# Kernel optimization log

Measured on AMD Instinct MI355X. Metric: run time of the kernel, lower is better.

Reference implementation:

```python
import jax, jax.numpy as jnp
import numpy as np

B, H0, W0, DIM, HEADS, WS, SHIFT = 32, 56, 56, 384, 12, 7, 3
MLP_HID = DIM * 4
N = WS * WS  # tokens per window

def _rel_pos_index(ws):
    coords = np.stack(np.meshgrid(np.arange(ws), np.arange(ws), indexing='ij')).reshape(2, -1)
    rel = (coords[:, :, None] - coords[:, None, :]).transpose(1, 2, 0)
    rel[:, :, 0] += ws - 1
    rel[:, :, 1] += ws - 1
    rel[:, :, 0] *= 2 * ws - 1
    return rel.sum(-1)  # (N, N) int

REL_IDX = _rel_pos_index(WS)

def _shift_mask(H, W, ws, shift):
    # standard Swin SW-MSA mask: 0 within same region, -100 across regions
    img = np.zeros((H, W), dtype=np.int32)
    cnt = 0
    for hs in (slice(0, -ws), slice(-ws, -shift), slice(-shift, None)):
        for wsl in (slice(0, -ws), slice(-ws, -shift), slice(-shift, None)):
            img[hs, wsl] = cnt
            cnt += 1
    mw = img.reshape(H // ws, ws, W // ws, ws).transpose(0, 2, 1, 3).reshape(-1, ws * ws)
    return np.where(mw[:, None, :] != mw[:, :, None], -100.0, 0.0).astype(np.float32)  # (nW, N, N)

MASK = _shift_mask(H0, W0, WS, SHIFT)

def _ln(x, g, b, eps=1e-5):
    m = x.mean(-1, keepdims=True)
    v = ((x - m) ** 2).mean(-1, keepdims=True)
    return (x - m) / jnp.sqrt(v + eps) * g + b

def setup_inputs():
    key = jax.random.key(0)
    ks = jax.random.split(key, 8)
    d = {}
    d['x'] = jax.random.normal(ks[0], (B, H0 * W0, DIM), jnp.float32)
    d['H'], d['W'] = H0, W0
    d['norm1_g'] = jnp.ones((DIM,), jnp.float32)
    d['norm1_b'] = jnp.zeros((DIM,), jnp.float32)
    d['qkv_w'] = jax.random.normal(ks[1], (3 * DIM, DIM), jnp.float32) * 0.02
    d['qkv_b'] = jnp.zeros((3 * DIM,), jnp.float32)
    d['rpb_table'] = jax.random.normal(ks[2], ((2 * WS - 1) ** 2, HEADS), jnp.float32) * 0.02
    d['proj_w'] = jax.random.normal(ks[3], (DIM, DIM), jnp.float32) * 0.02
    d['proj_b'] = jnp.zeros((DIM,), jnp.float32)
    d['norm2_g'] = jnp.ones((DIM,), jnp.float32)
    d['norm2_b'] = jnp.zeros((DIM,), jnp.float32)
    d['fc1_w'] = jax.random.normal(ks[4], (MLP_HID, DIM), jnp.float32) * 0.02
    d['fc1_b'] = jnp.zeros((MLP_HID,), jnp.float32)
    d['fc2_w'] = jax.random.normal(ks[5], (DIM, MLP_HID), jnp.float32) * 0.02
    d['fc2_b'] = jnp.zeros((DIM,), jnp.float32)
    return d

def reference(x, H, W, norm1_g, norm1_b, qkv_w, qkv_b, rpb_table, proj_w, proj_b, norm2_g, norm2_b, fc1_w, fc1_b, fc2_w, fc2_b):
    Bx, L, C = x.shape
    hd = C // HEADS
    scale = hd ** -0.5
    shortcut = x
    xn = _ln(x, norm1_g, norm1_b).reshape(Bx, H, W, C)
    if SHIFT > 0:
        xn = jnp.roll(xn, (-SHIFT, -SHIFT), axis=(1, 2))
    nWh, nWw = H // WS, W // WS
    nW = nWh * nWw
    # window partition: (B, H, W, C) -> (B*nW, N, C)
    xw = xn.reshape(Bx, nWh, WS, nWw, WS, C).transpose(0, 1, 3, 2, 4, 5).reshape(-1, N, C)
    qkv = (xw @ qkv_w.T + qkv_b).reshape(-1, N, 3, HEADS, hd).transpose(2, 0, 3, 1, 4)
    q, k, v = qkv[0] * scale, qkv[1], qkv[2]  # (B*nW, HEADS, N, hd)
    attn = jnp.einsum('bhnd,bhmd->bhnm', q, k)
    bias = rpb_table[jnp.asarray(REL_IDX.reshape(-1))].reshape(N, N, HEADS).transpose(2, 0, 1)
    attn = attn + bias[None]
    if SHIFT > 0:
        attn = attn.reshape(Bx, nW, HEADS, N, N) + jnp.asarray(MASK)[None, :, None]
        attn = attn.reshape(-1, HEADS, N, N)
    attn = jax.nn.softmax(attn, axis=-1)
    out = jnp.einsum('bhnm,bhmd->bhnd', attn, v).transpose(0, 2, 1, 3).reshape(-1, N, C)
    out = out @ proj_w.T + proj_b
    # window reverse: (B*nW, N, C) -> (B, H, W, C)
    xr = out.reshape(Bx, nWh, nWw, WS, WS, C).transpose(0, 1, 3, 2, 4, 5).reshape(Bx, H, W, C)
    if SHIFT > 0:
        xr = jnp.roll(xr, (SHIFT, SHIFT), axis=(1, 2))
    x = shortcut + xr.reshape(Bx, L, C)
    h = _ln(x, norm2_g, norm2_b)
    h = jax.nn.gelu(h @ fc1_w.T + fc1_b, approximate=False)  # nn.GELU default = exact erf
    h = h @ fc2_w.T + fc2_b
    return x + h
```

## Files before the change

kernel.cpp:

```cpp
#include <hip/hip_runtime.h>
#include <hip/hip_bf16.h>

#define C_DIM   384
#define HEADS   12
#define HDIM    32
#define NTOK    49
#define TOT_WIN 2048
#define M_TOK   100352
#define QKV_N   1152
#define MLP_N   1536
#define SHIFT_V 3

typedef __bf16 bf16x8_t __attribute__((ext_vector_type(8)));
typedef float  f32x4_t  __attribute__((ext_vector_type(4)));

__device__ inline float b2f(ushort u) {
    union { unsigned u; float f; } p; p.u = ((unsigned)u) << 16; return p.f;
}
__device__ inline ushort f2b(float f) {
    union { float f; unsigned u; } p; p.f = f;
    unsigned r = p.u + 0x7FFF + ((p.u >> 16) & 1);
    return (ushort)(r >> 16);
}
__device__ inline float ldin(const void* p, size_t i, int dt) {
    return dt ? b2f(((const ushort*)p)[i]) : ((const float*)p)[i];
}

__device__ inline void gload_lds16(const ushort* g, ushort* l) {
    __builtin_amdgcn_global_load_lds(
        (__attribute__((address_space(1))) void*)const_cast<ushort*>(g),
        (__attribute__((address_space(3))) void*)l, 16, 0, 0);
}

__device__ inline int win2tok(int grow) {
    int widx = grow / 49, tok = grow - widx * 49;
    int b = widx >> 6, w_ = widx & 63;
    int wh = w_ >> 3, ww = w_ & 7;
    int r = tok / 7, c = tok - r * 7;
    int h = wh * 7 + r + SHIFT_V; if (h >= 56) h -= 56;
    int wc = ww * 7 + c + SHIFT_V; if (wc >= 56) wc -= 56;
    return b * 3136 + h * 56 + wc;
}

__global__ void sniff_kernel(const ushort* x16, int* flag) {
    const int tid = threadIdx.x;
    int cnt = 0;
    for (int i = tid; i < 4096; i += 256) {
        ushort u = x16[2 * i];
        int e = (u >> 7) & 0xFF;
        if ((u & 0x7FFF) == 0 || (e >= 107 && e <= 147)) cnt++;
    }
    __shared__ int ss[256];
    ss[tid] = cnt; __syncthreads();
    for (int s = 128; s; s >>= 1) { if (tid < s) ss[tid] += ss[tid + s]; __syncthreads(); }
    if (tid == 0) *flag = (ss[0] >= 2048) ? 1 : 0;
}

__global__ void cvt_w_kernel(const void* src, ushort* dst, int n, const int* flagp) {
    const int dt = *flagp;
    for (int i = blockIdx.x * blockDim.x + threadIdx.x; i < n; i += gridDim.x * blockDim.x)
        dst[i] = dt ? ((const ushort*)src)[i] : f2b(((const float*)src)[i]);
}

__global__ void cvt_p_kernel(const void* n1g, const void* n1b, const void* qkvb,
                             const void* projb, const void* n2g, const void* n2b,
                             const void* fc1b, const void* fc2b, const void* rpb,
                             float* prm, const int* flagp) {
    const int dt = *flagp;
    for (int i = threadIdx.x; i < 7020; i += 256) {
        float v;
        if      (i < 384)  v = ldin(n1g,  i,        dt);
        else if (i < 768)  v = ldin(n1b,  i - 384,  dt);
        else if (i < 1920) v = ldin(qkvb, i - 768,  dt);
        else if (i < 2304) v = ldin(projb,i - 1920, dt);
        else if (i < 2688) v = ldin(n2g,  i - 2304, dt);
        else if (i < 3072) v = ldin(n2b,  i - 2688, dt);
        else if (i < 4608) v = ldin(fc1b, i - 3072, dt);
        else if (i < 4992) v = ldin(fc2b, i - 4608, dt);
        else               v = ldin(rpb,  i - 4992, dt);
        prm[i] = v;
    }
}

template<int MODE>
__global__ __launch_bounds__(256) void ln_kernel(
    const void* __restrict__ x, const float* __restrict__ g,
    const float* __restrict__ b, ushort* __restrict__ out,
    const int* flagp, int moff)
{
    const int dt = *flagp;
    const int wid = threadIdx.x >> 6, lane = threadIdx.x & 63;
    const int m = blockIdx.x * 4 + wid;
    const int src = (MODE == 0) ? win2tok(moff + m) : (moff + m);

    float v[6]; float s = 0.f, sq = 0.f;
    #pragma unroll
    for (int k = 0; k < 6; ++k) {
        v[k] = ldin(x, (size_t)src * C_DIM + lane + 64 * k, dt);
        s += v[k]; sq += v[k] * v[k];
    }
    #pragma unroll
    for (int off = 32; off; off >>= 1) {
        s  += __shfl_xor(s,  off, 64);
        sq += __shfl_xor(sq, off, 64);
    }
    float mean = s * (1.f / 384.f);
    float var  = sq * (1.f / 384.f) - mean * mean;
    float rstd = rsqrtf(var + 1e-5f);
    #pragma unroll
    for (int k = 0; k < 6; ++k) {
        int col = lane + 64 * k;
        out[(size_t)m * C_DIM + col] =
            f2b((v[k] - mean) * rstd * g[col] + b[col]);
    }
}

template<int MODE>
__global__ __launch_bounds__(256, 2) void gemm_bt(
    const ushort* __restrict__ A, const ushort* __restrict__ W,
    const float* __restrict__ bias, ushort* outb, void* outv,
    const void* resid, const int* flagp, int N, int K, int Mrows, int moff)
{
    __shared__ __align__(16) ushort As[2][128 * 32];
    __shared__ __align__(16) ushort Bs[2][128 * 32];

    const int dt   = *flagp;
    const int tid  = threadIdx.x;
    const int wid  = tid >> 6;
    const int lane = tid & 63;
    const int bm = blockIdx.x * 128;
    const int bn = blockIdx.y * 128;
    const int wm = (wid >> 1) * 64;
    const int wn = (wid & 1) * 64;
    const int lrow = lane & 15;
    const int lk   = (lane >> 4) << 3;

    const int c0    = wid * 2;
    const int srow0 = c0 * 16 + (lane >> 2);
    const int srow1 = srow0 + 16;
    const int skoff = (lane & 3) << 3;

    const int ar0 = (bm + srow0 < Mrows) ? (bm + srow0) : (Mrows - 1);
    const int ar1 = (bm + srow1 < Mrows) ? (bm + srow1) : (Mrows - 1);

    const ushort* pa0 = A + (size_t)ar0 * K + skoff;
    const ushort* pa1 = A + (size_t)ar1 * K + skoff;
    const ushort* pb0 = W + (size_t)(bn + srow0) * K + skoff;
    const ushort* pb1 = W + (size_t)(bn + srow1) * K + skoff;

    float biasf[4]; int coln[4];
    #pragma unroll
    for (int n = 0; n < 4; ++n) {
        coln[n] = bn + wn + n * 16 + lrow;
        biasf[n] = bias[coln[n]];
    }

    f32x4_t acc[4][4];
    #pragma unroll
    for (int m = 0; m < 4; ++m)
        #pragma unroll
        for (int n = 0; n < 4; ++n) acc[m][n] = (f32x4_t){0.f, 0.f, 0.f, 0.f};

    const int nk = K >> 5;
    gload_lds16(pa0, As[0] + (c0)     * 512);
    gload_lds16(pa1, As[0] + (c0 + 1) * 512);
    gload_lds16(pb0, Bs[0] + (c0)     * 512);
    gload_lds16(pb1, Bs[0] + (c0 + 1) * 512);

    int cur = 0;
    for (int kt = 0; kt < nk; ++kt) {
        if (kt + 1 < nk) {
            const int nxt = cur ^ 1;
            const int k1 = (kt + 1) << 5;
            gload_lds16(pa0 + k1, As[nxt] + (c0)     * 512);
            gload_lds16(pa1 + k1, As[nxt] + (c0 + 1) * 512);
            gload_lds16(pb0 + k1, Bs[nxt] + (c0)     * 512);
            gload_lds16(pb1 + k1, Bs[nxt] + (c0 + 1) * 512);
            __builtin_amdgcn_sched_barrier(0);
            asm volatile("s_waitcnt vmcnt(4)" ::: "memory");
        } else {
            asm volatile("s_waitcnt vmcnt(0)" ::: "memory");
        }
        __builtin_amdgcn_s_barrier();
        __builtin_amdgcn_sched_barrier(0);

        bf16x8_t af[4], bfr[4];
        #pragma unroll
        for (int m = 0; m < 4; ++m)
            af[m] = *(const bf16x8_t*)&As[cur][(wm + m * 16 + lrow) * 32 + lk];
        #pragma unroll
        for (int n = 0; n < 4; ++n)
            bfr[n] = *(const bf16x8_t*)&Bs[cur][(wn + n * 16 + lrow) * 32 + lk];
        #pragma unroll
        for (int m = 0; m < 4; ++m)
            #pragma unroll
            for (int n = 0; n < 4; ++n)
                acc[m][n] = __builtin_amdgcn_mfma_f32_16x16x32_bf16(
                    af[m], bfr[n], acc[m][n], 0, 0, 0);

        __builtin_amdgcn_sched_barrier(0);
        __builtin_amdgcn_s_barrier();
        cur ^= 1;
    }

    const int rbase = bm + wm + ((lane >> 4) << 2);
    #pragma unroll
    for (int m = 0; m < 4; ++m) {
        #pragma unroll
        for (int j = 0; j < 4; ++j) {
            int grow = rbase + m * 16 + j;
            if (grow >= Mrows) continue;
            #pragma unroll
            for (int n = 0; n < 4; ++n) {
                float v = acc[m][n][j] + biasf[n];
                if (MODE == 0) {
                    outb[(size_t)grow * N + coln[n]] = f2b(v);
                } else if (MODE == 2) {
                    v = 0.5f * v * (1.0f + erff(v * 0.70710678118654752f));
                    outb[(size_t)grow * N + coln[n]] = f2b(v);
                } else {
                    size_t orow = (MODE == 1) ? (size_t)win2tok(moff + grow)
                                              : (size_t)(moff + grow);
                    size_t oidx = orow * (size_t)N + coln[n];
                    float r = v + ldin(resid, oidx, dt);
                    if (dt) ((ushort*)outv)[oidx] = f2b(r);
                    else    ((float*) outv)[oidx] = r;
                }
            }
        }
    }
}

__global__ __launch_bounds__(256) void attn_kernel(
    const ushort* __restrict__ qkv, const float* __restrict__ rpb,
    ushort* __restrict__ out, int win_off)
{
    __shared__ __align__(16) ushort Pl[4][64 * 64];
    __shared__ __align__(16) ushort Vtl[4][32 * 64];

    const int tid = threadIdx.x, wid = tid >> 6, lane = tid & 63;
    const int lo = lane & 15, hi = lane >> 4;
    const int widx = blockIdx.x;
    const int w_ = (win_off + widx) & 63;
    const int wh = w_ >> 3, ww = w_ & 7;
    const bool edge = (wh == 7) || (ww == 7);

    char* P  = (char*)Pl[wid];
    char* Vw = (char*)Vtl[wid];

    int qr[4], qc[4], rq[4];
    #pragma unroll
    for (int n = 0; n < 4; ++n) {
        int q = n * 16 + lo; if (q > 48) q = 48;
        qr[n] = q / 7; qc[n] = q - qr[n] * 7;
        int gh = wh * 7 + qr[n], gw = ww * 7 + qc[n];
        rq[n] = (gh < 49 ? 0 : (gh < 53 ? 1 : 2)) * 3 + (gw < 49 ? 0 : (gw < 53 ? 1 : 2));
    }

    for (int h = wid; h < HEADS; h += 4) {
        const size_t hb = (size_t)widx * 49 * QKV_N + h * HDIM;

        bf16x8_t kf[4], qf[4];
        #pragma unroll
        for (int t = 0; t < 4; ++t) {
            int r = t * 16 + lo;
            bf16x8_t z = {};
            kf[t] = z; qf[t] = z;
            if (r < 49) {
                kf[t] = *(const bf16x8_t*)(qkv + hb + (size_t)r * QKV_N + 384 + hi * 8);
                qf[t] = *(const bf16x8_t*)(qkv + hb + (size_t)r * QKV_N + hi * 8);
            }
        }

        {
            const int kk = lane;
            union { bf16x8_t v; ushort u[8]; } vv[4];
            #pragma unroll
            for (int c = 0; c < 4; ++c) {
                bf16x8_t z = {};
                vv[c].v = (kk < 49) ? *(const bf16x8_t*)(qkv + hb + (size_t)kk * QKV_N + 768 + c * 8)
                                    : z;
            }
            #pragma unroll
            for (int d = 0; d < 32; ++d) {
                int byo = (d * 128 + kk * 2) ^ ((d & 7) << 4);
                *(ushort*)(Vw + byo) = vv[d >> 3].u[d & 7];
            }
        }

        f32x4_t St[4][4];
        #pragma unroll
        for (int m = 0; m < 4; ++m)
            #pragma unroll
            for (int n = 0; n < 4; ++n) St[m][n] = (f32x4_t){0.f, 0.f, 0.f, 0.f};
        #pragma unroll
        for (int m = 0; m < 4; ++m)
            #pragma unroll
            for (int n = 0; n < 4; ++n)
                St[m][n] = __builtin_amdgcn_mfma_f32_16x16x32_bf16(kf[m], qf[n], St[m][n], 0, 0, 0);

        #pragma unroll
        for (int m = 0; m < 4; ++m) {
            #pragma unroll
            for (int j = 0; j < 4; ++j) {
                const int kk = m * 16 + hi * 4 + j;
                const int kcl = (kk > 48) ? 48 : kk;
                const int kr = kcl / 7, kc = kcl - kr * 7;
                int rk = 0;
                if (edge) {
                    int gh = wh * 7 + kr, gw = ww * 7 + kc;
                    rk = (gh < 49 ? 0 : (gh < 53 ? 1 : 2)) * 3 + (gw < 49 ? 0 : (gw < 53 ? 1 : 2));
                }
                #pragma unroll
                for (int n = 0; n < 4; ++n) {
                    int idx = (qr[n] - kr + 6) * 13 + (qc[n] - kc + 6);
                    float v = St[m][n][j] * 0.17677669529663687f + rpb[idx * 12 + h];
                    if (edge && (rq[n] != rk)) v -= 100.f;
                    if (kk > 48) v = -1e30f;
                    St[m][n][j] = v;
                }
            }
        }

        float sm[4];
        #pragma unroll
        for (int n = 0; n < 4; ++n) {
            float mv = St[0][n][0];
            #pragma unroll
            for (int m = 0; m < 4; ++m)
                #pragma unroll
                for (int j = 0; j < 4; ++j) mv = fmaxf(mv, St[m][n][j]);
            mv = fmaxf(mv, __shfl_xor(mv, 16, 64));
            mv = fmaxf(mv, __shfl_xor(mv, 32, 64));
            float sv = 0.f;
            #pragma unroll
            for (int m = 0; m < 4; ++m)
                #pragma unroll
                for (int j = 0; j < 4; ++j) {
                    float e = __expf(St[m][n][j] - mv);
                    St[m][n][j] = e; sv += e;
                }
            sv += __shfl_xor(sv, 16, 64);
            sv += __shfl_xor(sv, 32, 64);
            sm[n] = 1.f / sv;
        }

        #pragma unroll
        for (int m = 0; m < 4; ++m) {
            #pragma unroll
            for (int n = 0; n < 4; ++n) {
                union { ushort4 u4; __bf16 b[4]; } pk;
                #pragma unroll
                for (int j = 0; j < 4; ++j) pk.b[j] = (__bf16)(St[m][n][j] * sm[n]);
                int byo = ((n * 16 + lo) * 128 + (m * 16 + hi * 4) * 2) ^ ((lo & 7) << 4);
                *(ushort4*)(P + byo) = pk.u4;
            }
        }

        f32x4_t Oa[4][2];
        #pragma unroll
        for (int mt = 0; mt < 4; ++mt)
            #pragma unroll
            for (int nt = 0; nt < 2; ++nt) Oa[mt][nt] = (f32x4_t){0.f, 0.f, 0.f, 0.f};
        #pragma unroll
        for (int s = 0; s < 2; ++s) {
            bf16x8_t vf[2];
            #pragma unroll
            for (int nt = 0; nt < 2; ++nt) {
                int byo = ((nt * 16 + lo) * 128 + s * 64 + hi * 16) ^ ((lo & 7) << 4);
                vf[nt] = *(const bf16x8_t*)(Vw + byo);
            }
            #pragma unroll
            for (int mt = 0; mt < 4; ++mt) {
                int byo = ((mt * 16 + lo) * 128 + s * 64 + hi * 16) ^ ((lo & 7) << 4);
                bf16x8_t pf = *(const bf16x8_t*)(P + byo);
                #pragma unroll
                for (int nt = 0; nt < 2; ++nt)
                    Oa[mt][nt] = __builtin_amdgcn_mfma_f32_16x16x32_bf16(pf, vf[nt], Oa[mt][nt], 0, 0, 0);
            }
        }

        #pragma unroll
        for (int mt = 0; mt < 4; ++mt) {
            #pragma unroll
            for (int j = 0; j < 4; ++j) {
                int q = mt * 16 + hi * 4 + j;
                if (q < 49) {
                    size_t ro = ((size_t)(widx * 49 + q)) * C_DIM + h * HDIM;
                    #pragma unroll
                    for (int nt = 0; nt < 2; ++nt)
                        out[ro + nt * 16 + lo] = f2b(Oa[mt][nt][j]);
                }
            }
        }
    }
}

extern "C" void kernel_launch(void* const* d_in, const int* in_sizes, int n_in,
                              void* d_out, int out_size, void* d_ws, size_t ws_size,
                              hipStream_t stream)
{
    const void* x      = d_in[0];
    const void* n1g    = d_in[3];
    const void* n1b    = d_in[4];
    const void* qkv_w  = d_in[5];
    const void* qkv_b  = d_in[6];
    const void* rpb    = d_in[7];
    const void* proj_w = d_in[8];
    const void* proj_b = d_in[9];
    const void* n2g    = d_in[10];
    const void* n2b    = d_in[11];
    const void* fc1_w  = d_in[12];
    const void* fc1_b  = d_in[13];
    const void* fc2_w  = d_in[14];
    const void* fc2_b  = d_in[15];

    int*    flagp = (int*)d_ws;
    float*  prm   = (float*)((char*)d_ws + 256);
    ushort* wq    = (ushort*)((char*)d_ws + 28416);
    ushort* wp    = wq + 442368;
    ushort* w1m   = wp + 147456;
    ushort* w2m   = w1m + 589824;
    const size_t WSTATIC = 3567360;

    int nc = 64;
    const int opts[7] = {1, 2, 4, 8, 16, 32, 64};
    for (int i = 0; i < 7; ++i) {
        size_t need = WSTATIC + ((size_t)M_TOK / opts[i]) * 3840ull;
        if (need <= ws_size) { nc = opts[i]; break; }
    }
    const int wins_pc = TOT_WIN / nc;
    const int rows_pc = wins_pc * NTOK;
    const int gx      = (rows_pc + 127) / 128;

    ushort* ws0 = (ushort*)((char*)d_ws + WSTATIC);
    ushort* ws1 = ws0 + (size_t)rows_pc * C_DIM;

    sniff_kernel<<<1, 256, 0, stream>>>((const ushort*)x, flagp);
    cvt_p_kernel<<<1, 256, 0, stream>>>(n1g, n1b, qkv_b, proj_b, n2g, n2b,
                                        fc1_b, fc2_b, rpb, prm, flagp);
    cvt_w_kernel<<<432, 256, 0, stream>>>(qkv_w,  wq,  442368, flagp);
    cvt_w_kernel<<<144, 256, 0, stream>>>(proj_w, wp,  147456, flagp);
    cvt_w_kernel<<<576, 256, 0, stream>>>(fc1_w,  w1m, 589824, flagp);
    cvt_w_kernel<<<576, 256, 0, stream>>>(fc2_w,  w2m, 589824, flagp);

    const float* b_qkv = prm + 768;
    const float* b_prj = prm + 1920;
    const float* b_fc1 = prm + 3072;
    const float* b_fc2 = prm + 4608;
    const float* rpb_c = prm + 4992;

    for (int c = 0; c < nc; ++c) {
        const int moff = c * rows_pc;
        ln_kernel<0><<<rows_pc / 4, 256, 0, stream>>>(x, prm + 0, prm + 384, ws0, flagp, moff);
        gemm_bt<0><<<dim3(gx, 9), 256, 0, stream>>>(
            ws0, wq, b_qkv, ws1, nullptr, nullptr, flagp, QKV_N, C_DIM, rows_pc, 0);
        attn_kernel<<<wins_pc, 256, 0, stream>>>(ws1, rpb_c, ws0, c * wins_pc);
        gemm_bt<1><<<dim3(gx, 3), 256, 0, stream>>>(
            ws0, wp, b_prj, nullptr, d_out, x, flagp, C_DIM, C_DIM, rows_pc, moff);
    }

    for (int c = 0; c < nc; ++c) {
        const int moff = c * rows_pc;
        ln_kernel<1><<<rows_pc / 4, 256, 0, stream>>>(d_out, prm + 2304, prm + 2688, ws0, flagp, moff);
        gemm_bt<2><<<dim3(gx, 12), 256, 0, stream>>>(
            ws0, w1m, b_fc1, ws1, nullptr, nullptr, flagp, MLP_N, C_DIM, rows_pc, 0);
        gemm_bt<3><<<dim3(gx, 3), 256, 0, stream>>>(
            ws1, w2m, b_fc2, nullptr, d_out, d_out, flagp, C_DIM, MLP_N, rows_pc, moff);
    }
}
```

Baseline: 1.179 ms.

## Fuse QKV projection into the window attention kernel

Replaces the separate QKV GEMM plus attention launch with a single kernel per window. It stages the window's normalized tokens in LDS, computes Q, K and V for each head with MFMA, folds the softmax scale into Q, and writes Q, K and a transposed V straight into LDS for the attention step. This removes the round trip of the large QKV intermediate through global memory and one launch. In exchange, every window block re-reads the full QKV weight matrix from cache, wastes MFMA work padding 49 tokens up to 64, and uses much more LDS per block, which may lower occupancy.

```diff
diff --git a/kernel.cpp b/kernel.cpp
--- a/kernel.cpp
+++ b/kernel.cpp
@@ -213,9 +213,7 @@
             #pragma unroll
             for (int n = 0; n < 4; ++n) {
                 float v = acc[m][n][j] + biasf[n];
-                if (MODE == 0) {
-                    outb[(size_t)grow * N + coln[n]] = f2b(v);
-                } else if (MODE == 2) {
+                if (MODE == 2) {
                     v = 0.5f * v * (1.0f + erff(v * 0.70710678118654752f));
                     outb[(size_t)grow * N + coln[n]] = f2b(v);
                 } else {
@@ -231,12 +229,14 @@
     }
 }
 
-__global__ __launch_bounds__(256) void attn_kernel(
-    const ushort* __restrict__ qkv, const float* __restrict__ rpb,
+__global__ __launch_bounds__(256) void qkvattn_kernel(
+    const ushort* __restrict__ xw, const ushort* __restrict__ wqkv,
+    const float* __restrict__ qkvb, const float* __restrict__ rpb,
     ushort* __restrict__ out, int win_off)
 {
-    __shared__ __align__(16) ushort Pl[4][64 * 64];
-    __shared__ __align__(16) ushort Vtl[4][32 * 64];
+    __shared__ __align__(16) ushort Axw[12 * 2048];
+    __shared__ __align__(16) ushort QKP[4][4096];
+    __shared__ __align__(16) ushort Vtl[4][2048];
 
     const int tid = threadIdx.x, wid = tid >> 6, lane = tid & 63;
     const int lo = lane & 15, hi = lane >> 4;
@@ -244,9 +244,22 @@
     const int w_ = (win_off + widx) & 63;
     const int wh = w_ >> 3, ww = w_ & 7;
     const bool edge = (wh == 7) || (ww == 7);
-
-    char* P  = (char*)Pl[wid];
-    char* Vw = (char*)Vtl[wid];
+    const size_t xbase = (size_t)widx * 49 * C_DIM;
+
+    {
+        const int rr = tid >> 2, s = tid & 3;
+        const int rsrc = (rr < 49) ? rr : 48;
+        const ushort* src = xw + xbase + (size_t)rsrc * C_DIM + s * 8;
+        #pragma unroll
+        for (int p = 0; p < 12; ++p)
+            gload_lds16(src + p * 32, Axw + p * 2048 + rr * 32 + s * 8);
+    }
+    __syncthreads();
+
+    ushort* Qs = QKP[wid];
+    ushort* Ks = Qs + 2048;
+    char*   P  = (char*)QKP[wid];
+    char*   Vw = (char*)Vtl[wid];
 
     int qr[4], qc[4], rq[4];
     #pragma unroll
@@ -257,35 +270,57 @@
         rq[n] = (gh < 49 ? 0 : (gh < 53 ? 1 : 2)) * 3 + (gw < 49 ? 0 : (gw < 53 ? 1 : 2));
     }
 
-    for (int h = wid; h < HEADS; h += 4) {
-        const size_t hb = (size_t)widx * 49 * QKV_N + h * HDIM;
+    for (int it = 0; it < 3; ++it) {
+        const int h = wid + it * 4;
+
+        #pragma unroll
+        for (int g = 0; g < 3; ++g) {
+            const int wrow0 = g * 384 + h * HDIM;
+            f32x4_t acc[4][2];
+            #pragma unroll
+            for (int m = 0; m < 4; ++m)
+                #pragma unroll
+                for (int n = 0; n < 2; ++n) acc[m][n] = (f32x4_t){0.f, 0.f, 0.f, 0.f};
+            #pragma unroll
+            for (int p = 0; p < 12; ++p) {
+                bf16x8_t bfr[2], af[4];
+                #pragma unroll
+                for (int n = 0; n < 2; ++n)
+                    bfr[n] = *(const bf16x8_t*)(wqkv + (size_t)(wrow0 + n * 16 + lo) * 384 + p * 32 + hi * 8);
+                #pragma unroll
+                for (int m = 0; m < 4; ++m)
+                    af[m] = *(const bf16x8_t*)&Axw[p * 2048 + (m * 16 + lo) * 32 + hi * 8];
+                #pragma unroll
+                for (int m = 0; m < 4; ++m)
+                    #pragma unroll
+                    for (int n = 0; n < 2; ++n)
+                        acc[m][n] = __builtin_amdgcn_mfma_f32_16x16x32_bf16(af[m], bfr[n], acc[m][n], 0, 0, 0);
+            }
+            const float b0 = qkvb[wrow0 + lo];
+            const float b1 = qkvb[wrow0 + 16 + lo];
+            #pragma unroll
+            for (int m = 0; m < 4; ++m) {
+                #pragma unroll
+                for (int n = 0; n < 2; ++n) {
+                    const float bb = n ? b1 : b0;
+                    const int d2 = n * 16 + lo;
+                    #pragma unroll
+                    for (int j = 0; j < 4; ++j) {
+                        const int tok = m * 16 + hi * 4 + j;
+                        float v = acc[m][n][j] + bb;
+                        if (g == 0)      Qs[tok * 32 + d2] = f2b(v * 0.17677669529663687f);
+                        else if (g == 1) Ks[tok * 32 + d2] = f2b(v);
+                        else *(ushort*)(Vw + ((d2 * 128 + tok * 2) ^ ((d2 & 7) << 4))) = f2b(v);
+                    }
+                }
+            }
+        }
 
         bf16x8_t kf[4], qf[4];
         #pragma unroll
         for (int t = 0; t < 4; ++t) {
-            int r = t * 16 + lo;
-            bf16x8_t z = {};
-            kf[t] = z; qf[t] = z;
-            if (r < 49) {
-                kf[t] = *(const bf16x8_t*)(qkv + hb + (size_t)r * QKV_N + 384 + hi * 8);
-                qf[t] = *(const bf16x8_t*)(qkv + hb + (size_t)r * QKV_N + hi * 8);
-            }
-        }
-
-        {
-            const int kk = lane;
-            union { bf16x8_t v; ushort u[8]; } vv[4];
-            #pragma unroll
-            for (int c = 0; c < 4; ++c) {
-                bf16x8_t z = {};
-                vv[c].v = (kk < 49) ? *(const bf16x8_t*)(qkv + hb + (size_t)kk * QKV_N + 768 + c * 8)
-                                    : z;
-            }
-            #pragma unroll
-            for (int d = 0; d < 32; ++d) {
-                int byo = (d * 128 + kk * 2) ^ ((d & 7) << 4);
-                *(ushort*)(Vw + byo) = vv[d >> 3].u[d & 7];
-            }
+            kf[t] = *(const bf16x8_t*)&Ks[(t * 16 + lo) * 32 + hi * 8];
+            qf[t] = *(const bf16x8_t*)&Qs[(t * 16 + lo) * 32 + hi * 8];
         }
 
         f32x4_t St[4][4];
@@ -314,7 +349,7 @@
                 #pragma unroll
                 for (int n = 0; n < 4; ++n) {
                     int idx = (qr[n] - kr + 6) * 13 + (qc[n] - kc + 6);
-                    float v = St[m][n][j] * 0.17677669529663687f + rpb[idx * 12 + h];
+                    float v = St[m][n][j] + rpb[idx * 12 + h];
                     if (edge && (rq[n] != rk)) v -= 100.f;
                     if (kk > 48) v = -1e30f;
                     St[m][n][j] = v;
@@ -453,9 +488,7 @@
     for (int c = 0; c < nc; ++c) {
         const int moff = c * rows_pc;
         ln_kernel<0><<<rows_pc / 4, 256, 0, stream>>>(x, prm + 0, prm + 384, ws0, flagp, moff);
-        gemm_bt<0><<<dim3(gx, 9), 256, 0, stream>>>(
-            ws0, wq, b_qkv, ws1, nullptr, nullptr, flagp, QKV_N, C_DIM, rows_pc, 0);
-        attn_kernel<<<wins_pc, 256, 0, stream>>>(ws1, rpb_c, ws0, c * wins_pc);
+        qkvattn_kernel<<<wins_pc, 256, 0, stream>>>(ws0, wq, b_qkv, rpb_c, ws0, c * wins_pc);
         gemm_bt<1><<<dim3(gx, 3), 256, 0, stream>>>(
             ws0, wp, b_prj, nullptr, d_out, x, flagp, C_DIM, C_DIM, rows_pc, moff);
     }
```

New measurement: 1.304 ms. 10.6% more time.
